# Kernel optimization log

Hardware: AMD Instinct MI355X
Metric: run time of the kernel (lower is better)

Reference implementation:

```python
import jax, jax.numpy as jnp
import numpy as np

B, T, NC, D = 8, 4096, 2048, 1024  # batch, original_len, num_chunks, d_model


def setup_inputs() -> dict:
    key = jax.random.key(0)
    k1, k2, k3 = jax.random.split(key, 3)
    z = jax.random.normal(k1, (B, NC, D), dtype=jnp.float32)
    p = jax.random.uniform(k2, (B, T), dtype=jnp.float32)
    b = jax.random.randint(k3, (B, T), 0, 2, dtype=jnp.int32)
    return {"z": z, "p": p, "b": b, "original_len": T}


def reference(z, p, b, original_len):
    # z: [B, NC, D], p: [B, T], b: [B, T] boundary flags in {0,1}
    num_chunks = z.shape[1]
    # idx at time t = exclusive cumsum of b (idx advances AFTER copying z[idx]);
    # once idx >= num_chunks the torch loop uses z[:, -1], i.e. clamp to NC-1.
    idx = jnp.clip(jnp.cumsum(b, axis=1) - b, 0, num_chunks - 1)  # [B, T]
    upsampled = jnp.take_along_axis(z, idx[..., None], axis=1)    # [B, T, D]
    coef = p[..., None]                                           # [B, T, 1]
    rolled = jnp.roll(upsampled, shift=1, axis=1)
    smoothed = coef * upsampled + (1.0 - coef) * rolled
    smoothed = smoothed.at[:, 0].set(upsampled[:, 0])
    return smoothed
```

## Files before the change

### kernel.cpp

```cpp
#include <hip/hip_runtime.h>

#define BATCH 8
#define TLEN  4096
#define NCHUNK 2048
#define DMODEL 1024
#define ROWS_PER_BLOCK 16

__global__ void dechunk_scan_kernel(const int* __restrict__ bflag,
                                    int* __restrict__ idx) {
    const int batch = blockIdx.x;
    const int tid = threadIdx.x;
    const int* bb = bflag + (size_t)batch * TLEN;
    int* ii = idx + (size_t)batch * TLEN;

    const int base = tid * 16;
    int vals[16];
    int s = 0;
    const int4* bv = (const int4*)(bb + base);
#pragma unroll
    for (int k = 0; k < 4; ++k) {
        int4 v = bv[k];
        vals[4 * k + 0] = v.x; vals[4 * k + 1] = v.y;
        vals[4 * k + 2] = v.z; vals[4 * k + 3] = v.w;
        s += v.x + v.y + v.z + v.w;
    }

    __shared__ int sm[256];
    sm[tid] = s;
    __syncthreads();
#pragma unroll
    for (int off = 1; off < 256; off <<= 1) {
        int v = (tid >= off) ? sm[tid - off] : 0;
        __syncthreads();
        sm[tid] += v;
        __syncthreads();
    }
    int run = sm[tid] - s;

    int outv[16];
#pragma unroll
    for (int k = 0; k < 16; ++k) {
        outv[k] = min(run, NCHUNK - 1);
        run += vals[k];
    }
    int4* iv = (int4*)(ii + base);
#pragma unroll
    for (int k = 0; k < 4; ++k) {
        iv[k] = make_int4(outv[4 * k + 0], outv[4 * k + 1],
                          outv[4 * k + 2], outv[4 * k + 3]);
    }
}

__global__ void dechunk_smooth_kernel(const float* __restrict__ z,
                                      const float* __restrict__ p,
                                      const int* __restrict__ idx,
                                      float* __restrict__ out) {
    const int chunks_per_batch = TLEN / ROWS_PER_BLOCK;
    const int chunk = blockIdx.x;
    const int batch = chunk / chunks_per_batch;
    const int t0 = (chunk - batch * chunks_per_batch) * ROWS_PER_BLOCK;
    const int tid = threadIdx.x;
    const int bt0 = batch * TLEN + t0;

    __shared__ int lidx[ROWS_PER_BLOCK + 1];
    __shared__ float lp[ROWS_PER_BLOCK];
    if (tid < ROWS_PER_BLOCK + 1) {
        int g = bt0 - 1 + tid;
        lidx[tid] = idx[max(g, 0)];
    } else if (tid >= 64 && tid < 64 + ROWS_PER_BLOCK) {
        lp[tid - 64] = p[bt0 + (tid - 64)];
    }
    __syncthreads();

    const float* zb = z + (size_t)batch * NCHUNK * DMODEL;
    float4* outr = (float4*)(out + (size_t)bt0 * DMODEL);

    int last_i;
    float4 val;
    int j0 = 0;

    if (t0 == 0) {
        last_i = lidx[1];
        val = ((const float4*)(zb + (size_t)last_i * DMODEL))[tid];
        outr[tid] = val;
        j0 = 1;
    } else {
        last_i = lidx[0];
        val = ((const float4*)(zb + (size_t)last_i * DMODEL))[tid];
    }

    for (int j = j0; j < ROWS_PER_BLOCK; ++j) {
        const int ci = lidx[j + 1];
        float4 o;
        if (ci == last_i) {
            o = val;
        } else {
            float4 nv = ((const float4*)(zb + (size_t)ci * DMODEL))[tid];
            const float pv = lp[j];
            const float q = 1.0f - pv;
            o.x = pv * nv.x + q * val.x;
            o.y = pv * nv.y + q * val.y;
            o.z = pv * nv.z + q * val.z;
            o.w = pv * nv.w + q * val.w;
            val = nv;
            last_i = ci;
        }
        outr[j * (DMODEL / 4) + tid] = o;
    }
}

extern "C" void kernel_launch(void* const* d_in, const int* in_sizes, int n_in,
                              void* d_out, int out_size, void* d_ws, size_t ws_size,
                              hipStream_t stream) {
    const float* z = (const float*)d_in[0];
    const float* p = (const float*)d_in[1];
    const int* bflag = (const int*)d_in[2];
    float* out = (float*)d_out;
    int* idx = (int*)d_ws;

    dechunk_scan_kernel<<<BATCH, 256, 0, stream>>>(bflag, idx);
    dechunk_smooth_kernel<<<BATCH * (TLEN / ROWS_PER_BLOCK), 256, 0, stream>>>(
        z, p, idx, out);
}
```

Before: 42.20 us.

## Batch all row gathers up front in smooth kernel and use wave-shuffle scan

The smoothing kernel now issues all 17 row loads into a register array before computing, instead of a serial loop with data-dependent branches and loads. This exposes memory-level parallelism across rows, at the cost of redundant loads when consecutive indices repeat and higher register use. The scan kernel replaces the shared-memory Hillis-Steele scan, which needed many barriers, with wavefront shuffles plus a small per-wave offset pass. It also fixes the blend at equal indices to compute the formula directly, which gives the same result.

```diff
diff --git a/kernel.cpp b/kernel.cpp
--- a/kernel.cpp
+++ b/kernel.cpp
@@ -10,6 +10,8 @@
                                     int* __restrict__ idx) {
     const int batch = blockIdx.x;
     const int tid = threadIdx.x;
+    const int lane = tid & 63;
+    const int wid = tid >> 6;
     const int* bb = bflag + (size_t)batch * TLEN;
     int* ii = idx + (size_t)batch * TLEN;
 
@@ -25,17 +27,22 @@
         s += v.x + v.y + v.z + v.w;
     }
 
-    __shared__ int sm[256];
-    sm[tid] = s;
+    int incl = s;
+#pragma unroll
+    for (int off = 1; off < 64; off <<= 1) {
+        int n = __shfl_up(incl, off, 64);
+        if (lane >= off) incl += n;
+    }
+
+    __shared__ int wsum[4];
+    if (lane == 63) wsum[wid] = incl;
     __syncthreads();
+    int woff = 0;
 #pragma unroll
-    for (int off = 1; off < 256; off <<= 1) {
-        int v = (tid >= off) ? sm[tid - off] : 0;
-        __syncthreads();
-        sm[tid] += v;
-        __syncthreads();
-    }
-    int run = sm[tid] - s;
+    for (int w = 0; w < 4; ++w)
+        woff += (w < wid) ? wsum[w] : 0;
+
+    int run = woff + incl - s;
 
     int outv[16];
 #pragma unroll
@@ -67,43 +74,34 @@
     if (tid < ROWS_PER_BLOCK + 1) {
         int g = bt0 - 1 + tid;
         lidx[tid] = idx[max(g, 0)];
-    } else if (tid >= 64 && tid < 64 + ROWS_PER_BLOCK) {
-        lp[tid - 64] = p[bt0 + (tid - 64)];
+    } else if (tid >= 32 && tid < 32 + ROWS_PER_BLOCK) {
+        lp[tid - 32] = p[bt0 + (tid - 32)];
     }
     __syncthreads();
 
     const float* zb = z + (size_t)batch * NCHUNK * DMODEL;
     float4* outr = (float4*)(out + (size_t)bt0 * DMODEL);
 
-    int last_i;
-    float4 val;
-    int j0 = 0;
-
-    if (t0 == 0) {
-        last_i = lidx[1];
-        val = ((const float4*)(zb + (size_t)last_i * DMODEL))[tid];
-        outr[tid] = val;
-        j0 = 1;
-    } else {
-        last_i = lidx[0];
-        val = ((const float4*)(zb + (size_t)last_i * DMODEL))[tid];
+    float4 v[ROWS_PER_BLOCK + 1];
+#pragma unroll
+    for (int j = 0; j <= ROWS_PER_BLOCK; ++j) {
+        v[j] = ((const float4*)(zb + (size_t)lidx[j] * DMODEL))[tid];
     }
 
-    for (int j = j0; j < ROWS_PER_BLOCK; ++j) {
-        const int ci = lidx[j + 1];
+#pragma unroll
+    for (int j = 0; j < ROWS_PER_BLOCK; ++j) {
+        float4 a = v[j + 1];
         float4 o;
-        if (ci == last_i) {
-            o = val;
+        if (j == 0 && t0 == 0) {
+            o = a;
         } else {
-            float4 nv = ((const float4*)(zb + (size_t)ci * DMODEL))[tid];
+            float4 r = v[j];
             const float pv = lp[j];
             const float q = 1.0f - pv;
-            o.x = pv * nv.x + q * val.x;
-            o.y = pv * nv.y + q * val.y;
-            o.z = pv * nv.z + q * val.z;
-            o.w = pv * nv.w + q * val.w;
-            val = nv;
-            last_i = ci;
+            o.x = pv * a.x + q * r.x;
+            o.y = pv * a.y + q * r.y;
+            o.z = pv * a.z + q * r.z;
+            o.w = pv * a.w + q * r.w;
         }
         outr[j * (DMODEL / 4) + tid] = o;
     }
```

Measured after the change: 41.44 us. No clear change (-1.8%).
